# Kernel tuning notes

Measured on AMD Instinct MI355X. Metric: run time of the kernel, lower is better.

## Reference

```python
import jax, jax.numpy as jnp
import numpy as np

EPS = 1e-9
C, Hd, Wd = 3, 64, 64  # input_dimensions[1:]

def setup_inputs() -> dict:
    key = jax.random.key(0)
    ks = jax.random.split(key, 8)
    S, B = 8, 512
    num_digits, num_style, num_hidden, bott, num_pixels = 10, 50, 512, 160, C * Hd * Wd
    return {
        "digits": jax.random.uniform(ks[0], (S, B, num_digits), dtype=jnp.float32),
        "styles": jax.random.normal(ks[1], (S, B, num_style), dtype=jnp.float32),
        "images": jax.random.uniform(ks[2], (S, B, C, Hd, Wd), dtype=jnp.float32),
        "W_h": jax.random.normal(ks[3], (num_digits + num_style, num_hidden), dtype=jnp.float32) * 0.05,
        "b_h": jnp.zeros((num_hidden,), jnp.float32),
        "W1": jax.random.normal(ks[4], (num_hidden, bott), dtype=jnp.float32) * 0.05,
        "b1": jnp.zeros((bott,), jnp.float32),
        "W2": jax.random.normal(ks[5], (bott, num_pixels), dtype=jnp.float32) * 0.05,
        "b2": jnp.zeros((num_pixels,), jnp.float32),
    }

def reference(digits, styles, images, W_h, b_h, W1, b1, W2, b2):
    # dec_hidden: Linear + ReLU, fully batched over [S, B]
    h = jax.nn.relu(jnp.concatenate([digits, styles], axis=-1) @ W_h + b_h)  # [S,B,Hn]
    # hidden_pass (original loops per-sample; here a single batched GEMM chain)
    t = jax.nn.selu(h @ W1 + b1)                 # [S,B,160]
    x_hat = jax.nn.sigmoid(t @ W2 + b2)          # [S,B,P]
    S, B, _ = x_hat.shape
    images_mean = x_hat.reshape(S, B, C, Hd, Wd)
    # eps-guarded BCE-style log-likelihood loss, summed over last dim only
    loss = -(jnp.log(images_mean + EPS) * images
             + jnp.log(1.0 - images_mean + EPS) * (1.0 - images)).sum(-1)  # [S,B,C,Hd]
    return loss
```

## Files before the change

### kernel.cpp

```cpp
#include <hip/hip_runtime.h>
#include <hip/hip_bf16.h>
#include <math.h>


#define SELU_SCALE 1.0507009873554804934193349852946f
#define SELU_ALPHA 1.6732632423543772848170429916717f

typedef __attribute__((ext_vector_type(8))) short bf16x8;
typedef __attribute__((ext_vector_type(4))) float f32x4;

static __device__ __forceinline__ short f2bf(float x) {
    __hip_bfloat16 h = __float2bfloat16(x);
    short s;
    __builtin_memcpy(&s, &h, 2);
    return s;
}

__global__ __launch_bounds__(256) void w2_pack_kernel(
    const float* __restrict__ W2,
    __hip_bfloat16* __restrict__ w2f)
{
    __shared__ float tile[32][64];
    const int colBase = blockIdx.x * 64;
    const int kkBase  = blockIdx.y * 32;
    const int tid = threadIdx.x;

    for (int i = tid; i < 32 * 64; i += 256)
        tile[i >> 6][i & 63] = W2[(size_t)(kkBase + (i >> 6)) * 12288 + colBase + (i & 63)];
    __syncthreads();

    const int c16 = tid >> 6;
    const int lane = tid & 63;
    const int lr = lane & 15, lh = lane >> 4;

    bf16x8 v;
#pragma unroll
    for (int j = 0; j < 8; ++j)
        v[j] = f2bf(tile[lh * 8 + j][c16 * 16 + lr]);

    const size_t chunk = (size_t)(blockIdx.x * 4 + c16) * 5 + blockIdx.y;
    *(bf16x8*)((short*)w2f + chunk * 512 + lane * 8) = v;
}

__global__ __launch_bounds__(512) void dec_fused_kernel(
    const float* __restrict__ digits,
    const float* __restrict__ styles,
    const float* __restrict__ Wh,
    const float* __restrict__ bh,
    const float* __restrict__ W1,
    const float* __restrict__ b1,
    __hip_bfloat16* __restrict__ tf)
{
    __shared__ float cat_s[16][60];
    __shared__ float h_s[16 * 512];
    __shared__ float t_s[16][161];

    const int tid = threadIdx.x;
    const int rowBase = blockIdx.x * 16;

    for (int i = tid; i < 16 * 60; i += 512) {
        const int r = i / 60, k = i % 60;
        const int row = rowBase + r;
        cat_s[r][k] = (k < 10) ? digits[row * 10 + k]
                               : styles[row * 50 + (k - 10)];
    }
    __syncthreads();

    {
        float acc[16];
        const float bias = bh[tid];
#pragma unroll
        for (int r = 0; r < 16; ++r) acc[r] = bias;
        for (int k = 0; k < 60; ++k) {
            const float w = Wh[k * 512 + tid];
#pragma unroll
            for (int r = 0; r < 16; ++r) acc[r] = fmaf(cat_s[r][k], w, acc[r]);
        }
#pragma unroll
        for (int r = 0; r < 16; ++r)
            h_s[r * 512 + tid] = fmaxf(acc[r], 0.0f);
    }
    __syncthreads();

    if (tid < 320) {
        const int rh = (tid >= 160) ? 1 : 0;
        const int col = tid - rh * 160;
        const int r0 = rh * 8;
        float acc[8];
        const float bias = b1[col];
#pragma unroll
        for (int r = 0; r < 8; ++r) acc[r] = bias;

#pragma unroll 4
        for (int k = 0; k < 512; k += 4) {
            const float w0 = W1[(size_t)(k + 0) * 160 + col];
            const float w1 = W1[(size_t)(k + 1) * 160 + col];
            const float w2 = W1[(size_t)(k + 2) * 160 + col];
            const float w3 = W1[(size_t)(k + 3) * 160 + col];
#pragma unroll
            for (int r = 0; r < 8; ++r) {
                const float4 hv = *(const float4*)&h_s[(r0 + r) * 512 + k];
                float a = acc[r];
                a = fmaf(hv.x, w0, a);
                a = fmaf(hv.y, w1, a);
                a = fmaf(hv.z, w2, a);
                a = fmaf(hv.w, w3, a);
                acc[r] = a;
            }
        }
#pragma unroll
        for (int r = 0; r < 8; ++r) {
            const float z = acc[r];
            const float s = (z > 0.0f) ? (SELU_SCALE * z)
                                       : (SELU_SCALE * SELU_ALPHA * expm1f(z));
            t_s[r0 + r][col] = s;
        }
    }
    __syncthreads();

    if (tid < 320) {
        const int kk = tid >> 6;
        const int l = tid & 63;
        const int lr = l & 15, lh = l >> 4;
        bf16x8 v;
#pragma unroll
        for (int j = 0; j < 8; ++j)
            v[j] = f2bf(t_s[lr][kk * 32 + lh * 8 + j]);
        *(bf16x8*)((short*)tf + ((size_t)blockIdx.x * 5 + kk) * 512 + l * 8) = v;
    }
}

__global__ __launch_bounds__(256, 3) void out_loss_mfma_kernel(
    const __hip_bfloat16* __restrict__ tf,
    const __hip_bfloat16* __restrict__ w2f,
    const float* __restrict__ b2,
    const float* __restrict__ images,
    float* __restrict__ out)
{
    __shared__ short w2s[20 * 512];
    __shared__ float ims[4][2048];

    const int tid = threadIdx.x;
    const int lane = tid & 63;
    const int wv = tid >> 6;
    const int rowBase = blockIdx.y * 128 + wv * 32;
    const int colBase = blockIdx.x * 64;
    const int lr = lane & 15;
    const int lh = lane >> 4;

    const short* wfb = (const short*)w2f;
    const short* tfb = (const short*)tf;
    const char* imb = (const char*)images;

    const int r16base = rowBase >> 4;
    bf16x8 bT[5][2];
#pragma unroll
    for (int kk = 0; kk < 5; ++kk)
#pragma unroll
        for (int r = 0; r < 2; ++r)
            bT[kk][r] = *(const bf16x8*)(tfb
                + ((size_t)(r16base + r) * 5 + kk) * 512 + lane * 8);
    float4 bc[4];
#pragma unroll
    for (int c = 0; c < 4; ++c)
        bc[c] = *(const float4*)(b2 + colBase + c * 16 + lh * 4);

    {
        const size_t chunkBase = (size_t)blockIdx.x * 20;
#pragma unroll
        for (int tch = 0; tch < 5; ++tch) {
            const int cw = wv + tch * 4;
            __builtin_amdgcn_global_load_lds(
                (const uint32_t*)(wfb + (chunkBase + cw) * 512 + lane * 8),
                (uint32_t*)&w2s[cw * 512], 16, 0, 0);
        }
    }
    {
        const int rsub = lane >> 4;
        const int m = lane & 15;
#pragma unroll
        for (int w = 0; w < 8; ++w) {
            const int r = w * 4 + rsub;
            const size_t gb = (size_t)(rowBase + r) * 49152 + (size_t)colBase * 4
                            + (size_t)((16 * m) ^ ((r & 15) << 4));
            __builtin_amdgcn_global_load_lds((const uint32_t*)(imb + gb),
                (uint32_t*)&ims[wv][w * 256], 16, 0, 0);
        }
    }

    asm volatile("s_waitcnt vmcnt(8)" ::: "memory");
    __builtin_amdgcn_sched_barrier(0);
    __builtin_amdgcn_s_barrier();

    f32x4 acc[4][2] = {};
#pragma unroll
    for (int kk = 0; kk < 5; ++kk) {
        bf16x8 aW[4];
#pragma unroll
        for (int c = 0; c < 4; ++c)
            aW[c] = *(const bf16x8*)&w2s[(c * 5 + kk) * 512 + lane * 8];
#pragma unroll
        for (int c = 0; c < 4; ++c)
#pragma unroll
            for (int r = 0; r < 2; ++r)
                acc[c][r] = __builtin_amdgcn_mfma_f32_16x16x32_bf16(
                    aW[c], bT[kk][r], acc[c][r], 0, 0, 0);
    }

    asm volatile("s_waitcnt vmcnt(0)" ::: "memory");
    __builtin_amdgcn_sched_barrier(0);

    const float* myq = ims[wv];
#pragma unroll
    for (int rw = 0; rw < 2; ++rw) {
        float mx = 0.f;
        float pr = 1.f;
        float zi = 0.f;
#pragma unroll
        for (int c = 0; c < 4; ++c) {
            const int fidx = (rw * 16 + lr) * 64 + ((lh * 4 + c * 16) ^ (lr << 2));
            const float4 im4 = *(const float4*)&myq[fidx];
            const float imv[4] = {im4.x, im4.y, im4.z, im4.w};
            const float bcv[4] = {bc[c].x, bc[c].y, bc[c].z, bc[c].w};
#pragma unroll
            for (int j = 0; j < 4; ++j) {
                const float z = acc[c][rw][j] + bcv[j];
                mx += fmaxf(z, 0.0f);
                pr *= 1.0f + __expf(-fabsf(z));
                zi = fmaf(z, imv[j], zi);
            }
        }
        float part = mx + __logf(pr) - zi;

        part += __shfl_xor(part, 16);
        part += __shfl_xor(part, 32);

        if (lane < 16)
            out[(size_t)(rowBase + rw * 16 + lane) * 192 + blockIdx.x] = part;
    }
}

extern "C" void kernel_launch(void* const* d_in, const int* in_sizes, int n_in,
                              void* d_out, int out_size, void* d_ws, size_t ws_size,
                              hipStream_t stream) {
    const float* digits = (const float*)d_in[0];
    const float* styles = (const float*)d_in[1];
    const float* images = (const float*)d_in[2];
    const float* Wh     = (const float*)d_in[3];
    const float* bh     = (const float*)d_in[4];
    const float* W1     = (const float*)d_in[5];
    const float* b1     = (const float*)d_in[6];
    const float* W2     = (const float*)d_in[7];
    const float* b2     = (const float*)d_in[8];
    float* out = (float*)d_out;

    __hip_bfloat16* w2f = (__hip_bfloat16*)d_ws;
    __hip_bfloat16* tf  = w2f + (size_t)12288 * 160;

    dim3 gridP(192, 5);
    w2_pack_kernel<<<gridP, 256, 0, stream>>>(W2, w2f);

    dec_fused_kernel<<<256, 512, 0, stream>>>(digits, styles, Wh, bh, W1, b1, tf);

    dim3 grid3(192, 32);
    out_loss_mfma_kernel<<<grid3, 256, 0, stream>>>(tf, w2f, b2, images, out);
}
```

Before: 85.66 us.

## Merge W2 packing and decoder MLP into one producer launch; split image wait

Combines the W2 bf16 packing kernel and the decoder hidden/bottleneck kernel into a single 736-block launch. The first 256 blocks run the MLP and the rest pack W2 tiles, two per block. This removes one kernel launch and lets the two independent producers run concurrently. The output kernel also splits its final image-load wait so the first row-group's loss starts after only half of the image loads have landed. The merged kernel uses a larger shared-memory footprint for every block, which may lower occupancy for the packing blocks.

```diff
diff --git a/kernel.cpp b/kernel.cpp
--- a/kernel.cpp
+++ b/kernel.cpp
@@ -16,117 +16,120 @@
     return s;
 }
 
-__global__ __launch_bounds__(256) void w2_pack_kernel(
-    const float* __restrict__ W2,
-    __hip_bfloat16* __restrict__ w2f)
-{
-    __shared__ float tile[32][64];
-    const int colBase = blockIdx.x * 64;
-    const int kkBase  = blockIdx.y * 32;
-    const int tid = threadIdx.x;
-
-    for (int i = tid; i < 32 * 64; i += 256)
-        tile[i >> 6][i & 63] = W2[(size_t)(kkBase + (i >> 6)) * 12288 + colBase + (i & 63)];
-    __syncthreads();
-
-    const int c16 = tid >> 6;
-    const int lane = tid & 63;
-    const int lr = lane & 15, lh = lane >> 4;
-
-    bf16x8 v;
-#pragma unroll
-    for (int j = 0; j < 8; ++j)
-        v[j] = f2bf(tile[lh * 8 + j][c16 * 16 + lr]);
-
-    const size_t chunk = (size_t)(blockIdx.x * 4 + c16) * 5 + blockIdx.y;
-    *(bf16x8*)((short*)w2f + chunk * 512 + lane * 8) = v;
-}
-
-__global__ __launch_bounds__(512) void dec_fused_kernel(
+__global__ __launch_bounds__(512) void producer_kernel(
     const float* __restrict__ digits,
     const float* __restrict__ styles,
     const float* __restrict__ Wh,
     const float* __restrict__ bh,
     const float* __restrict__ W1,
     const float* __restrict__ b1,
+    const float* __restrict__ W2,
+    __hip_bfloat16* __restrict__ w2f,
     __hip_bfloat16* __restrict__ tf)
 {
-    __shared__ float cat_s[16][60];
-    __shared__ float h_s[16 * 512];
-    __shared__ float t_s[16][161];
-
+    __shared__ __align__(16) char smem[46912];
     const int tid = threadIdx.x;
-    const int rowBase = blockIdx.x * 16;
-
-    for (int i = tid; i < 16 * 60; i += 512) {
-        const int r = i / 60, k = i % 60;
-        const int row = rowBase + r;
-        cat_s[r][k] = (k < 10) ? digits[row * 10 + k]
-                               : styles[row * 50 + (k - 10)];
-    }
-    __syncthreads();
-
-    {
-        float acc[16];
-        const float bias = bh[tid];
-#pragma unroll
-        for (int r = 0; r < 16; ++r) acc[r] = bias;
-        for (int k = 0; k < 60; ++k) {
-            const float w = Wh[k * 512 + tid];
-#pragma unroll
-            for (int r = 0; r < 16; ++r) acc[r] = fmaf(cat_s[r][k], w, acc[r]);
-        }
-#pragma unroll
-        for (int r = 0; r < 16; ++r)
-            h_s[r * 512 + tid] = fmaxf(acc[r], 0.0f);
-    }
-    __syncthreads();
-
-    if (tid < 320) {
-        const int rh = (tid >= 160) ? 1 : 0;
-        const int col = tid - rh * 160;
-        const int r0 = rh * 8;
-        float acc[8];
-        const float bias = b1[col];
-#pragma unroll
-        for (int r = 0; r < 8; ++r) acc[r] = bias;
+
+    if (blockIdx.x < 256) {
+        float (*cat_s)[60] = (float(*)[60])smem;
+        float* h_s = (float*)(smem + 3840);
+        float (*t_s)[161] = (float(*)[161])(smem + 3840 + 32768);
+        const int rowBase = blockIdx.x * 16;
+
+        for (int i = tid; i < 16 * 60; i += 512) {
+            const int r = i / 60, k = i % 60;
+            const int row = rowBase + r;
+            cat_s[r][k] = (k < 10) ? digits[row * 10 + k]
+                                   : styles[row * 50 + (k - 10)];
+        }
+        __syncthreads();
+
+        {
+            float acc[16];
+            const float bias = bh[tid];
+#pragma unroll
+            for (int r = 0; r < 16; ++r) acc[r] = bias;
+            for (int k = 0; k < 60; ++k) {
+                const float w = Wh[k * 512 + tid];
+#pragma unroll
+                for (int r = 0; r < 16; ++r) acc[r] = fmaf(cat_s[r][k], w, acc[r]);
+            }
+#pragma unroll
+            for (int r = 0; r < 16; ++r)
+                h_s[r * 512 + tid] = fmaxf(acc[r], 0.0f);
+        }
+        __syncthreads();
+
+        if (tid < 320) {
+            const int rh = (tid >= 160) ? 1 : 0;
+            const int col = tid - rh * 160;
+            const int r0 = rh * 8;
+            float acc[8];
+            const float bias = b1[col];
+#pragma unroll
+            for (int r = 0; r < 8; ++r) acc[r] = bias;
 
 #pragma unroll 4
-        for (int k = 0; k < 512; k += 4) {
-            const float w0 = W1[(size_t)(k + 0) * 160 + col];
-            const float w1 = W1[(size_t)(k + 1) * 160 + col];
-            const float w2 = W1[(size_t)(k + 2) * 160 + col];
-            const float w3 = W1[(size_t)(k + 3) * 160 + col];
+            for (int k = 0; k < 512; k += 4) {
+                const float w0 = W1[(size_t)(k + 0) * 160 + col];
+                const float w1 = W1[(size_t)(k + 1) * 160 + col];
+                const float w2 = W1[(size_t)(k + 2) * 160 + col];
+                const float w3 = W1[(size_t)(k + 3) * 160 + col];
+#pragma unroll
+                for (int r = 0; r < 8; ++r) {
+                    const float4 hv = *(const float4*)&h_s[(r0 + r) * 512 + k];
+                    float a = acc[r];
+                    a = fmaf(hv.x, w0, a);
+                    a = fmaf(hv.y, w1, a);
+                    a = fmaf(hv.z, w2, a);
+                    a = fmaf(hv.w, w3, a);
+                    acc[r] = a;
+                }
+            }
 #pragma unroll
             for (int r = 0; r < 8; ++r) {
-                const float4 hv = *(const float4*)&h_s[(r0 + r) * 512 + k];
-                float a = acc[r];
-                a = fmaf(hv.x, w0, a);
-                a = fmaf(hv.y, w1, a);
-                a = fmaf(hv.z, w2, a);
-                a = fmaf(hv.w, w3, a);
-                acc[r] = a;
-            }
-        }
-#pragma unroll
-        for (int r = 0; r < 8; ++r) {
-            const float z = acc[r];
-            const float s = (z > 0.0f) ? (SELU_SCALE * z)
-                                       : (SELU_SCALE * SELU_ALPHA * expm1f(z));
-            t_s[r0 + r][col] = s;
-        }
-    }
-    __syncthreads();
-
-    if (tid < 320) {
-        const int kk = tid >> 6;
-        const int l = tid & 63;
-        const int lr = l & 15, lh = l >> 4;
+                const float z = acc[r];
+                const float s = (z > 0.0f) ? (SELU_SCALE * z)
+                                           : (SELU_SCALE * SELU_ALPHA * expm1f(z));
+                t_s[r0 + r][col] = s;
+            }
+        }
+        __syncthreads();
+
+        if (tid < 320) {
+            const int kk = tid >> 6;
+            const int l = tid & 63;
+            const int lr = l & 15, lh = l >> 4;
+            bf16x8 v;
+#pragma unroll
+            for (int j = 0; j < 8; ++j)
+                v[j] = f2bf(t_s[lr][kk * 32 + lh * 8 + j]);
+            *(bf16x8*)((short*)tf + ((size_t)blockIdx.x * 5 + kk) * 512 + l * 8) = v;
+        }
+    } else {
+        float (*tile)[64] = (float(*)[64])(smem + (tid >> 8) * 8192);
+        const int p = (blockIdx.x - 256) * 2 + (tid >> 8);
+        const int t256 = tid & 255;
+        const int bx = p / 5, by = p % 5;
+        const int colBase = bx * 64;
+        const int kBase = by * 32;
+
+        for (int i = t256; i < 32 * 64; i += 256)
+            tile[i >> 6][i & 63] =
+                W2[(size_t)(kBase + (i >> 6)) * 12288 + colBase + (i & 63)];
+        __syncthreads();
+
+        const int c16 = t256 >> 6;
+        const int lane = t256 & 63;
+        const int lr = lane & 15, lh = lane >> 4;
+
         bf16x8 v;
 #pragma unroll
         for (int j = 0; j < 8; ++j)
-            v[j] = f2bf(t_s[lr][kk * 32 + lh * 8 + j]);
-        *(bf16x8*)((short*)tf + ((size_t)blockIdx.x * 5 + kk) * 512 + l * 8) = v;
+            v[j] = f2bf(tile[lh * 8 + j][c16 * 16 + lr]);
+
+        const size_t chunk = (size_t)(bx * 4 + c16) * 5 + by;
+        *(bf16x8*)((short*)w2f + chunk * 512 + lane * 8) = v;
     }
 }
 
@@ -207,12 +210,16 @@
                     aW[c], bT[kk][r], acc[c][r], 0, 0, 0);
     }
 
-    asm volatile("s_waitcnt vmcnt(0)" ::: "memory");
-    __builtin_amdgcn_sched_barrier(0);
-
     const float* myq = ims[wv];
 #pragma unroll
     for (int rw = 0; rw < 2; ++rw) {
+        if (rw == 0) {
+            asm volatile("s_waitcnt vmcnt(4)" ::: "memory");
+        } else {
+            asm volatile("s_waitcnt vmcnt(0)" ::: "memory");
+        }
+        __builtin_amdgcn_sched_barrier(0);
+
         float mx = 0.f;
         float pr = 1.f;
         float zi = 0.f;
@@ -257,10 +264,8 @@
     __hip_bfloat16* w2f = (__hip_bfloat16*)d_ws;
     __hip_bfloat16* tf  = w2f + (size_t)12288 * 160;
 
-    dim3 gridP(192, 5);
-    w2_pack_kernel<<<gridP, 256, 0, stream>>>(W2, w2f);
-
-    dec_fused_kernel<<<256, 512, 0, stream>>>(digits, styles, Wh, bh, W1, b1, tf);
+    producer_kernel<<<736, 512, 0, stream>>>(digits, styles, Wh, bh, W1, b1,
+                                             W2, w2f, tf);
 
     dim3 grid3(192, 32);
     out_loss_mfma_kernel<<<grid3, 256, 0, stream>>>(tf, w2f, b2, images, out);
```

Result: faster. 82.59 us (-3.6%).
